# Kernel optimization log

Measured on AMD Instinct MI355X. Metric: run time of the kernel, lower is better.

Reference implementation:

```python
import jax, jax.numpy as jnp
import numpy as np

B, N, D, H = 4, 2048, 1024, 16
DK = D // H
LAMBDA = 0.5


def _linear_params(key, fan_in, fan_out):
    kw, kb = jax.random.split(key)
    bound = 1.0 / np.sqrt(fan_in)
    W = jax.random.uniform(kw, (fan_in, fan_out), jnp.float32, -bound, bound)
    b = jax.random.uniform(kb, (fan_out,), jnp.float32, -bound, bound)
    return W, b


def setup_inputs() -> dict:
    key = jax.random.key(0)
    ks = jax.random.split(key, 10)
    x = jax.random.normal(ks[0], (B, N, D), jnp.float32)
    # binary DAG-like adjacency (sparse-ish)
    causal_graph = jax.random.bernoulli(ks[1], 0.05, (N, N)).astype(jnp.float32)
    # differentiable backdoor mask: exp(-lambda*|Z|), 0 where no valid backdoor set
    Z = jax.random.randint(ks[2], (N, N), 0, 6).astype(jnp.float32)
    exists = jax.random.bernoulli(ks[3], 0.8, (N, N)).astype(jnp.float32)
    backdoor_mask = jnp.exp(-LAMBDA * Z) * exists
    Wq, bq = _linear_params(ks[4], D, D)
    Wk, bk = _linear_params(ks[5], D, D)
    Wc, bc = _linear_params(ks[6], N, D)  # W_cause: n_variables -> d_model
    We, be = _linear_params(ks[7], N, D)  # W_effect: n_variables -> d_model
    Wv, bv = _linear_params(ks[8], D, D)
    Wo, bo = _linear_params(ks[9], D, D)
    return dict(x=x, causal_graph=causal_graph, backdoor_mask=backdoor_mask,
                Wq=Wq, bq=bq, Wk=Wk, bk=bk, Wc=Wc, bc=bc, We=We, be=be,
                Wv=Wv, bv=bv, Wo=Wo, bo=bo)


def reference(x, causal_graph, backdoor_mask, Wq, bq, Wk, bk, Wc, bc, We, be, Wv, bv, Wo, bo):
    # Formula 5: asymmetric causal Q/K projections
    Q = x @ Wq + bq + (causal_graph @ Wc + bc)[None]        # [B,N,D]
    K = x @ Wk + bk + (causal_graph.T @ We + be)[None]      # [B,N,D]
    V = x @ Wv + bv                                          # [B,N,D]
    Qh = Q.reshape(B, N, H, DK)
    Kh = K.reshape(B, N, H, DK)
    Vh = V.reshape(B, N, H, DK)
    scores = jnp.einsum('bihd,bjhd->bhij', Qh, Kh) / np.sqrt(DK).astype(np.float32)
    # backdoor mask is MULTIPLICATIVE on raw scores (pre-softmax)
    scores = scores * backdoor_mask[None, None]
    attn = jax.nn.softmax(scores, axis=-1)                  # [B,H,N,N]
    out = jnp.einsum('bhij,bjhd->bihd', attn, Vh).reshape(B, N, D)
    return out @ Wo + bo
```

## Files before the change

### kernel.cpp

```cpp
#include <hip/hip_runtime.h>
#include <hip/hip_bf16.h>

#define BB 4
#define NN 2048
#define DD 1024
#define HH 16

using bf16 = __hip_bfloat16;
typedef __attribute__((ext_vector_type(8))) short bf16x8s;
typedef __attribute__((ext_vector_type(4))) float f32x4;

#define GLOAD_LDS16(gp, lp)                                                   \
  __builtin_amdgcn_global_load_lds(                                           \
      (const __attribute__((address_space(1))) void*)(gp),                    \
      (__attribute__((address_space(3))) void*)(lp), 16, 0, 0)

__global__ void cast_f32_bf16(const float* __restrict__ in, bf16* __restrict__ out, int n) {
  int i = (blockIdx.x * blockDim.x + threadIdx.x) * 4;
  if (i >= n) return;
  float4 v = *reinterpret_cast<const float4*>(in + i);
  ushort4 o;
  bf16 t0 = __float2bfloat16(v.x); o.x = *reinterpret_cast<unsigned short*>(&t0);
  bf16 t1 = __float2bfloat16(v.y); o.y = *reinterpret_cast<unsigned short*>(&t1);
  bf16 t2 = __float2bfloat16(v.z); o.z = *reinterpret_cast<unsigned short*>(&t2);
  bf16 t3 = __float2bfloat16(v.w); o.w = *reinterpret_cast<unsigned short*>(&t3);
  *reinterpret_cast<ushort4*>(out + i) = o;
}

__device__ __forceinline__ void transpose_tile(const float* __restrict__ in,
                                               bf16* __restrict__ out, int R, int C) {
  __shared__ float t[32][33];
  int c0 = blockIdx.x * 32, r0 = blockIdx.y * 32;
  int tx = threadIdx.x, ty = threadIdx.y;
#pragma unroll
  for (int i = 0; i < 4; i++)
    t[ty + i * 8][tx] = in[(size_t)(r0 + ty + i * 8) * C + c0 + tx];
  __syncthreads();
#pragma unroll
  for (int i = 0; i < 4; i++)
    out[(size_t)(c0 + ty + i * 8) * R + r0 + tx] = __float2bfloat16(t[tx][ty + i * 8]);
}

__global__ void transpose_cast(const float* __restrict__ in, bf16* __restrict__ out, int R, int C) {
  transpose_tile(in, out, R, C);
}

__global__ void transpose_cast4(const float* __restrict__ W0, const float* __restrict__ W1,
                                const float* __restrict__ W2, const float* __restrict__ W3,
                                bf16* __restrict__ O0, bf16* __restrict__ O1,
                                bf16* __restrict__ O2, bf16* __restrict__ O3) {
  const float* in; bf16* out;
  switch (blockIdx.z) {
    case 0: in = W0; out = O0; break;
    case 1: in = W1; out = O1; break;
    case 2: in = W2; out = O2; break;
    default: in = W3; out = O3; break;
  }
  transpose_tile(in, out, DD, DD);
}

__global__ void transpose_v(const bf16* __restrict__ Vb, bf16* __restrict__ Vt) {
  __shared__ short t[32][33];
  int bh = blockIdx.z; int b = bh >> 4, h = bh & 15;
  int n0 = blockIdx.x * 32, d0 = blockIdx.y * 32;
  int tx = threadIdx.x, ty = threadIdx.y;
#pragma unroll
  for (int i = 0; i < 4; i++)
    t[ty + i * 8][tx] = reinterpret_cast<const short*>(Vb)[
        (size_t)(b * NN + n0 + ty + i * 8) * DD + h * 64 + d0 + tx];
  __syncthreads();
#pragma unroll
  for (int i = 0; i < 4; i++)
    reinterpret_cast<short*>(Vt)[(size_t)(bh * 64 + d0 + ty + i * 8) * NN + n0 + tx] =
        t[tx][ty + i * 8];
}

template <int OUT_BF16, int HAS_ROWADD>
__device__ __forceinline__ void gemm_tile(
    const bf16* __restrict__ A, const bf16* __restrict__ BT, void* __restrict__ Cout,
    const float* __restrict__ bias, const float* __restrict__ rowadd,
    int Nc, int K, float scale, int brow, int bcol, short* As, short* Bs) {
  const int tid = threadIdx.x;
  const int l = tid & 63, w = tid >> 6;
  const int wr = (w >> 1) * 64, wc = (w & 1) * 64;
  const int lr = l & 15, lg = l >> 4;
  const int swz = lr & 7;
  f32x4 acc[4][4] = {};
  for (int k0 = 0; k0 < K; k0 += 64) {
#pragma unroll
    for (int i = 0; i < 4; i++) {
      int c = i * 256 + tid;
      int row = c >> 3, gch = (c & 7) ^ (row & 7);
      short* lA = As + (size_t)(i * 256 + w * 64) * 8;
      GLOAD_LDS16(A + (size_t)(brow + row) * K + k0 + gch * 8, lA);
      short* lB = Bs + (size_t)(i * 256 + w * 64) * 8;
      GLOAD_LDS16(BT + (size_t)(bcol + row) * K + k0 + gch * 8, lB);
    }
    __syncthreads();
#pragma unroll
    for (int t = 0; t < 2; t++) {
      bf16x8s a[4], bfr[4];
#pragma unroll
      for (int m = 0; m < 4; m++)
        a[m] = *reinterpret_cast<const bf16x8s*>(
            &As[(wr + m * 16 + lr) * 64 + ((t * 4 + lg) ^ swz) * 8]);
#pragma unroll
      for (int n = 0; n < 4; n++)
        bfr[n] = *reinterpret_cast<const bf16x8s*>(
            &Bs[(wc + n * 16 + lr) * 64 + ((t * 4 + lg) ^ swz) * 8]);
#pragma unroll
      for (int m = 0; m < 4; m++)
#pragma unroll
        for (int n = 0; n < 4; n++)
          acc[m][n] = __builtin_amdgcn_mfma_f32_16x16x32_bf16(a[m], bfr[n], acc[m][n], 0, 0, 0);
    }
    __syncthreads();
  }
#pragma unroll
  for (int m = 0; m < 4; m++) {
#pragma unroll
    for (int n = 0; n < 4; n++) {
      int col = bcol + wc + n * 16 + lr;
      float bv = bias[col];
#pragma unroll
      for (int r = 0; r < 4; r++) {
        int row = brow + wr + m * 16 + lg * 4 + r;
        float v = acc[m][n][r] + bv;
        if (HAS_ROWADD) v += rowadd[(size_t)(row & (NN - 1)) * Nc + col];
        v *= scale;
        if (OUT_BF16)
          reinterpret_cast<bf16*>(Cout)[(size_t)row * Nc + col] = __float2bfloat16(v);
        else
          reinterpret_cast<float*>(Cout)[(size_t)row * Nc + col] = v;
      }
    }
  }
}

template <int OUT_BF16, int HAS_ROWADD>
__global__ __launch_bounds__(256) void gemm_bt(
    const bf16* __restrict__ A, const bf16* __restrict__ BT, void* __restrict__ Cout,
    const float* __restrict__ bias, const float* __restrict__ rowadd,
    int M, int Nc, int K, float scale) {
  __shared__ short As[128 * 64];
  __shared__ short Bs[128 * 64];
  const int nbx = gridDim.x;
  const int nwg = nbx * gridDim.y;
  const int wg = blockIdx.y * nbx + blockIdx.x;
  const int swg = (wg & 7) * (nwg >> 3) + (wg >> 3);
  const int bxi = swg % nbx, byi = swg / nbx;
  gemm_tile<OUT_BF16, HAS_ROWADD>(A, BT, Cout, bias, rowadd, Nc, K, scale,
                                  byi * 128, bxi * 128, As, Bs);
}

__global__ __launch_bounds__(256) void gemm_dual(
    const bf16* __restrict__ A0, const bf16* __restrict__ B0, float* __restrict__ C0,
    const float* __restrict__ bias0,
    const bf16* __restrict__ A1, const bf16* __restrict__ B1, float* __restrict__ C1,
    const float* __restrict__ bias1, int Nc, int K) {
  __shared__ short As[128 * 64];
  __shared__ short Bs[128 * 64];
  const int nbx = gridDim.x;
  const int nwg = nbx * gridDim.y;
  const int wg = blockIdx.y * nbx + blockIdx.x;
  const int swg = (wg & 7) * (nwg >> 3) + (wg >> 3);
  const int bxi = swg % nbx, byi = swg / nbx;
  if (blockIdx.z == 0)
    gemm_tile<0, 0>(A0, B0, C0, bias0, nullptr, Nc, K, 1.0f, byi * 128, bxi * 128, As, Bs);
  else
    gemm_tile<0, 0>(A1, B1, C1, bias1, nullptr, Nc, K, 1.0f, byi * 128, bxi * 128, As, Bs);
}

__global__ __launch_bounds__(512, 4) void attn_k(
    const bf16* __restrict__ Qb, const bf16* __restrict__ Kb, const bf16* __restrict__ Vt,
    const float* __restrict__ mask, bf16* __restrict__ Ob) {
  constexpr int PPAD = 72;
  __shared__ short Ks[64 * 64];
  __shared__ short Vts[64 * 64];
  __shared__ short Ps[8][16 * PPAD];
  const int tid = threadIdx.x;
  const int wg = blockIdx.x;
  const int x = wg & 7, i = wg >> 3;
  const int b = x >> 1;
  const int h = ((x & 1) << 3) | (i & 7);
  const int q0 = ((i >> 3) & 15) * 128;
  const int l = tid & 63, w = tid >> 6;
  const int lr = l & 15, lg = l >> 4, lk = lg * 8;
  const int swz = lr & 7;

  const size_t qoff = (size_t)(b * NN + q0 + w * 16 + lr) * DD + h * 64;
  bf16x8s qf0 = *reinterpret_cast<const bf16x8s*>(Qb + qoff + lk);
  bf16x8s qf1 = *reinterpret_cast<const bf16x8s*>(Qb + qoff + 32 + lk);

  f32x4 acc[4] = {};
  float mrun = -1e30f, lrun = 0.f;

  const size_t kbase = (size_t)b * NN * DD + h * 64;
  const size_t vbase = (size_t)(b * HH + h) * 64 * NN;
  const float* mptr = mask + (size_t)(q0 + w * 16 + lr) * NN + lg * 4;

  const int r0 = tid >> 3, ch0 = tid & 7;
  const bf16* kg0 = Kb + kbase + (size_t)r0 * DD + ch0 * 8;
  const bf16* vg0 = Vt + vbase + (size_t)r0 * NN + ch0 * 8;
  short* kw0 = &Ks[r0 * 64 + (ch0 ^ (r0 & 7)) * 8];
  short* vw0 = &Vts[r0 * 64 + (ch0 ^ (r0 & 7)) * 8];

  uint4 kr0, vr0;
  kr0 = *reinterpret_cast<const uint4*>(kg0);
  vr0 = *reinterpret_cast<const uint4*>(vg0);

  for (int jt = 0; jt < NN; jt += 64) {
    __syncthreads();
    *reinterpret_cast<uint4*>(kw0) = kr0;
    *reinterpret_cast<uint4*>(vw0) = vr0;
    float4 m0 = *reinterpret_cast<const float4*>(mptr + jt + 0);
    float4 m1 = *reinterpret_cast<const float4*>(mptr + jt + 16);
    float4 m2 = *reinterpret_cast<const float4*>(mptr + jt + 32);
    float4 m3 = *reinterpret_cast<const float4*>(mptr + jt + 48);
    if (jt + 64 < NN) {
      kr0 = *reinterpret_cast<const uint4*>(kg0 + (size_t)(jt + 64) * DD);
      vr0 = *reinterpret_cast<const uint4*>(vg0 + jt + 64);
    }
    __syncthreads();

    f32x4 s[4];
#pragma unroll
    for (int jj = 0; jj < 4; jj++) {
      bf16x8s k0 = *reinterpret_cast<const bf16x8s*>(
          &Ks[(jj * 16 + lr) * 64 + ((0 + lg) ^ swz) * 8]);
      bf16x8s k1 = *reinterpret_cast<const bf16x8s*>(
          &Ks[(jj * 16 + lr) * 64 + ((4 + lg) ^ swz) * 8]);
      f32x4 z = {0.f, 0.f, 0.f, 0.f};
      z = __builtin_amdgcn_mfma_f32_16x16x32_bf16(k0, qf0, z, 0, 0, 0);
      s[jj] = __builtin_amdgcn_mfma_f32_16x16x32_bf16(k1, qf1, z, 0, 0, 0);
    }

    float lv[4][4];
    lv[0][0] = s[0][0] * m0.x; lv[0][1] = s[0][1] * m0.y;
    lv[0][2] = s[0][2] * m0.z; lv[0][3] = s[0][3] * m0.w;
    lv[1][0] = s[1][0] * m1.x; lv[1][1] = s[1][1] * m1.y;
    lv[1][2] = s[1][2] * m1.z; lv[1][3] = s[1][3] * m1.w;
    lv[2][0] = s[2][0] * m2.x; lv[2][1] = s[2][1] * m2.y;
    lv[2][2] = s[2][2] * m2.z; lv[2][3] = s[2][3] * m2.w;
    lv[3][0] = s[3][0] * m3.x; lv[3][1] = s[3][1] * m3.y;
    lv[3][2] = s[3][2] * m3.z; lv[3][3] = s[3][3] * m3.w;

    float mx0 = fmaxf(fmaxf(lv[0][0], lv[0][1]), fmaxf(lv[0][2], lv[0][3]));
    float mx1 = fmaxf(fmaxf(lv[1][0], lv[1][1]), fmaxf(lv[1][2], lv[1][3]));
    float mx2 = fmaxf(fmaxf(lv[2][0], lv[2][1]), fmaxf(lv[2][2], lv[2][3]));
    float mx3 = fmaxf(fmaxf(lv[3][0], lv[3][1]), fmaxf(lv[3][2], lv[3][3]));
    float mx = fmaxf(fmaxf(mx0, mx1), fmaxf(mx2, mx3));
    mx = fmaxf(mx, __shfl_xor(mx, 16, 64));
    mx = fmaxf(mx, __shfl_xor(mx, 32, 64));

    if (__any(mx > mrun + 11.0f)) {
      float mnew = fmaxf(mrun, mx);
      float sc = __builtin_amdgcn_exp2f(mrun - mnew);
      mrun = mnew;
      lrun *= sc;
#pragma unroll
      for (int s4 = 0; s4 < 4; s4++)
#pragma unroll
        for (int r = 0; r < 4; r++) acc[s4][r] *= sc;
    }

    short* Pw = &Ps[w][0];
    float rs = 0.f;
#pragma unroll
    for (int jj = 0; jj < 4; jj++) {
      float p0 = __builtin_amdgcn_exp2f(lv[jj][0] - mrun);
      float p1 = __builtin_amdgcn_exp2f(lv[jj][1] - mrun);
      float p2 = __builtin_amdgcn_exp2f(lv[jj][2] - mrun);
      float p3 = __builtin_amdgcn_exp2f(lv[jj][3] - mrun);
      rs += (p0 + p1) + (p2 + p3);
      ushort4 pk;
      bf16 b0 = __float2bfloat16(p0); pk.x = *reinterpret_cast<unsigned short*>(&b0);
      bf16 b1 = __float2bfloat16(p1); pk.y = *reinterpret_cast<unsigned short*>(&b1);
      bf16 b2 = __float2bfloat16(p2); pk.z = *reinterpret_cast<unsigned short*>(&b2);
      bf16 b3 = __float2bfloat16(p3); pk.w = *reinterpret_cast<unsigned short*>(&b3);
      *reinterpret_cast<ushort4*>(&Pw[lr * PPAD + jj * 16 + lg * 4]) = pk;
    }
    rs += __shfl_xor(rs, 16, 64);
    rs += __shfl_xor(rs, 32, 64);
    lrun += rs;

    asm volatile("s_waitcnt lgkmcnt(0)" ::: "memory");
    __builtin_amdgcn_sched_barrier(0);

    bf16x8s pb0 = *reinterpret_cast<const bf16x8s*>(&Pw[lr * PPAD + lk]);
    bf16x8s pb1 = *reinterpret_cast<const bf16x8s*>(&Pw[lr * PPAD + 32 + lk]);
#pragma unroll
    for (int s4 = 0; s4 < 4; s4++) {
      bf16x8s v0 = *reinterpret_cast<const bf16x8s*>(
          &Vts[(s4 * 16 + lr) * 64 + ((0 + lg) ^ swz) * 8]);
      bf16x8s v1 = *reinterpret_cast<const bf16x8s*>(
          &Vts[(s4 * 16 + lr) * 64 + ((4 + lg) ^ swz) * 8]);
      acc[s4] = __builtin_amdgcn_mfma_f32_16x16x32_bf16(v0, pb0, acc[s4], 0, 0, 0);
      acc[s4] = __builtin_amdgcn_mfma_f32_16x16x32_bf16(v1, pb1, acc[s4], 0, 0, 0);
    }
  }

  float rl = __builtin_amdgcn_rcpf(lrun);
  const size_t orow = (size_t)(b * NN + q0 + w * 16 + lr) * DD + h * 64;
#pragma unroll
  for (int s4 = 0; s4 < 4; s4++) {
    ushort4 o;
    bf16 b0 = __float2bfloat16(acc[s4][0] * rl); o.x = *reinterpret_cast<unsigned short*>(&b0);
    bf16 b1 = __float2bfloat16(acc[s4][1] * rl); o.y = *reinterpret_cast<unsigned short*>(&b1);
    bf16 b2 = __float2bfloat16(acc[s4][2] * rl); o.z = *reinterpret_cast<unsigned short*>(&b2);
    bf16 b3 = __float2bfloat16(acc[s4][3] * rl); o.w = *reinterpret_cast<unsigned short*>(&b3);
    *reinterpret_cast<ushort4*>(reinterpret_cast<unsigned short*>(Ob) + orow + s4 * 16 + lg * 4) = o;
  }
}

extern "C" void kernel_launch(void* const* d_in, const int* in_sizes, int n_in,
                              void* d_out, int out_size, void* d_ws, size_t ws_size,
                              hipStream_t stream) {
  (void)in_sizes; (void)n_in; (void)out_size; (void)ws_size;
  const float* x    = (const float*)d_in[0];
  const float* cg   = (const float*)d_in[1];
  const float* mask = (const float*)d_in[2];
  const float* Wq   = (const float*)d_in[3];
  const float* bq   = (const float*)d_in[4];
  const float* Wk   = (const float*)d_in[5];
  const float* bk   = (const float*)d_in[6];
  const float* Wc   = (const float*)d_in[7];
  const float* bc   = (const float*)d_in[8];
  const float* We   = (const float*)d_in[9];
  const float* be   = (const float*)d_in[10];
  const float* Wv   = (const float*)d_in[11];
  const float* bv   = (const float*)d_in[12];
  const float* Wo   = (const float*)d_in[13];
  const float* bo   = (const float*)d_in[14];

  auto MB = [](size_t m) { return m << 20; };
  char* ws = (char*)d_ws;
  bf16* xb   = (bf16*)(ws + MB(0));
  bf16* WqT  = (bf16*)(ws + MB(16));
  bf16* WkT  = (bf16*)(ws + MB(18));
  bf16* WvT  = (bf16*)(ws + MB(20));
  bf16* WoT  = (bf16*)(ws + MB(22));
  float* cq  = (float*)(ws + MB(24));
  float* ck  = (float*)(ws + MB(32));
  bf16* Qb   = (bf16*)(ws + MB(40));
  bf16* Kb   = (bf16*)(ws + MB(56));
  bf16* Vb   = (bf16*)(ws + MB(72));
  bf16* Vt   = (bf16*)(ws + MB(88));
  bf16* Ob   = (bf16*)(ws + MB(72));
  bf16* WcT  = (bf16*)(ws + MB(40));
  bf16* WeT  = (bf16*)(ws + MB(44));
  bf16* cgb  = (bf16*)(ws + MB(48));
  bf16* cgT  = (bf16*)(ws + MB(56));

  cast_f32_bf16<<<dim3(BB * NN * DD / 4 / 256), 256, 0, stream>>>(x, xb, BB * NN * DD);
  cast_f32_bf16<<<dim3(NN * NN / 4 / 256), 256, 0, stream>>>(cg, cgb, NN * NN);
  dim3 tb(32, 8);
  transpose_cast4<<<dim3(DD / 32, DD / 32, 4), tb, 0, stream>>>(
      Wq, Wk, Wv, Wo, WqT, WkT, WvT, WoT);
  transpose_cast<<<dim3(DD / 32, NN / 32), tb, 0, stream>>>(Wc, WcT, NN, DD);
  transpose_cast<<<dim3(DD / 32, NN / 32), tb, 0, stream>>>(We, WeT, NN, DD);
  transpose_cast<<<dim3(NN / 32, NN / 32), tb, 0, stream>>>(cg, cgT, NN, NN);

  gemm_dual<<<dim3(DD / 128, NN / 128, 2), 256, 0, stream>>>(
      cgb, WcT, cq, bc, cgT, WeT, ck, be, DD, NN);
  gemm_bt<1, 1><<<dim3(DD / 128, BB * NN / 128), 256, 0, stream>>>(
      xb, WqT, Qb, bq, cq, BB * NN, DD, DD, 0.125f * 1.4426950408889634f);
  gemm_bt<1, 1><<<dim3(DD / 128, BB * NN / 128), 256, 0, stream>>>(
      xb, WkT, Kb, bk, ck, BB * NN, DD, DD, 1.0f);
  gemm_bt<1, 0><<<dim3(DD / 128, BB * NN / 128), 256, 0, stream>>>(
      xb, WvT, Vb, bv, nullptr, BB * NN, DD, DD, 1.0f);

  transpose_v<<<dim3(NN / 32, 2, BB * HH), tb, 0, stream>>>(Vb, Vt);

  attn_k<<<dim3(NN / 128 * HH * BB), 512, 0, stream>>>(Qb, Kb, Vt, mask, Ob);

  gemm_bt<0, 0><<<dim3(DD / 128, BB * NN / 128), 256, 0, stream>>>(
      Ob, WoT, (float*)d_out, bo, nullptr, BB * NN, DD, DD, 1.0f);
}
```

Before: 315.8 us.

## Double attention query tile per block and fuse causal-graph prep kernels

Attention blocks now run 1024 threads (16 waves) over 256 query rows. Each K/V tile loaded into LDS is therefore reused by twice as many waves, and half the threads stage K while the other half stage V. MFMA sections are wrapped in s_setprio to favour matrix issue. The preprocessing also fuses the causal-graph cast and its transpose into one kernel, and merges the two Wc/We transposes into a single launch. The risks are fewer blocks (512), which hurts load balance and tail, and register pressure under launch_bounds(1024, 8).

```diff
diff --git a/kernel.cpp b/kernel.cpp
--- a/kernel.cpp
+++ b/kernel.cpp
@@ -41,10 +41,6 @@
     out[(size_t)(c0 + ty + i * 8) * R + r0 + tx] = __float2bfloat16(t[tx][ty + i * 8]);
 }
 
-__global__ void transpose_cast(const float* __restrict__ in, bf16* __restrict__ out, int R, int C) {
-  transpose_tile(in, out, R, C);
-}
-
 __global__ void transpose_cast4(const float* __restrict__ W0, const float* __restrict__ W1,
                                 const float* __restrict__ W2, const float* __restrict__ W3,
                                 bf16* __restrict__ O0, bf16* __restrict__ O1,
@@ -57,6 +53,30 @@
     default: in = W3; out = O3; break;
   }
   transpose_tile(in, out, DD, DD);
+}
+
+__global__ void transpose_cast2(const float* __restrict__ W0, const float* __restrict__ W1,
+                                bf16* __restrict__ O0, bf16* __restrict__ O1) {
+  const float* in = blockIdx.z ? W1 : W0;
+  bf16* out = blockIdx.z ? O1 : O0;
+  transpose_tile(in, out, NN, DD);
+}
+
+__global__ void cg_prep(const float* __restrict__ in, bf16* __restrict__ outN,
+                        bf16* __restrict__ outT) {
+  __shared__ float t[32][33];
+  int c0 = blockIdx.x * 32, r0 = blockIdx.y * 32;
+  int tx = threadIdx.x, ty = threadIdx.y;
+#pragma unroll
+  for (int i = 0; i < 4; i++) {
+    float v = in[(size_t)(r0 + ty + i * 8) * NN + c0 + tx];
+    t[ty + i * 8][tx] = v;
+    outN[(size_t)(r0 + ty + i * 8) * NN + c0 + tx] = __float2bfloat16(v);
+  }
+  __syncthreads();
+#pragma unroll
+  for (int i = 0; i < 4; i++)
+    outT[(size_t)(c0 + ty + i * 8) * NN + r0 + tx] = __float2bfloat16(t[tx][ty + i * 8]);
 }
 
 __global__ void transpose_v(const bf16* __restrict__ Vb, bf16* __restrict__ Vt) {
@@ -171,19 +191,19 @@
     gemm_tile<0, 0>(A1, B1, C1, bias1, nullptr, Nc, K, 1.0f, byi * 128, bxi * 128, As, Bs);
 }
 
-__global__ __launch_bounds__(512, 4) void attn_k(
+__global__ __launch_bounds__(1024, 8) void attn_k(
     const bf16* __restrict__ Qb, const bf16* __restrict__ Kb, const bf16* __restrict__ Vt,
     const float* __restrict__ mask, bf16* __restrict__ Ob) {
   constexpr int PPAD = 72;
   __shared__ short Ks[64 * 64];
   __shared__ short Vts[64 * 64];
-  __shared__ short Ps[8][16 * PPAD];
+  __shared__ short Ps[16][16 * PPAD];
   const int tid = threadIdx.x;
   const int wg = blockIdx.x;
   const int x = wg & 7, i = wg >> 3;
   const int b = x >> 1;
   const int h = ((x & 1) << 3) | (i & 7);
-  const int q0 = ((i >> 3) & 15) * 128;
+  const int q0 = ((i >> 3) & 7) * 256;
   const int l = tid & 63, w = tid >> 6;
   const int lr = l & 15, lg = l >> 4, lk = lg * 8;
   const int swz = lr & 7;
@@ -199,31 +219,29 @@
   const size_t vbase = (size_t)(b * HH + h) * 64 * NN;
   const float* mptr = mask + (size_t)(q0 + w * 16 + lr) * NN + lg * 4;
 
-  const int r0 = tid >> 3, ch0 = tid & 7;
-  const bf16* kg0 = Kb + kbase + (size_t)r0 * DD + ch0 * 8;
-  const bf16* vg0 = Vt + vbase + (size_t)r0 * NN + ch0 * 8;
-  short* kw0 = &Ks[r0 * 64 + (ch0 ^ (r0 & 7)) * 8];
-  short* vw0 = &Vts[r0 * 64 + (ch0 ^ (r0 & 7)) * 8];
-
-  uint4 kr0, vr0;
-  kr0 = *reinterpret_cast<const uint4*>(kg0);
-  vr0 = *reinterpret_cast<const uint4*>(vg0);
+  const int sr = (tid & 511) >> 3, sch = tid & 7;
+  const bool isK = tid < 512;
+  const bf16* sg = isK ? (Kb + kbase + (size_t)sr * DD + sch * 8)
+                       : (Vt + vbase + (size_t)sr * NN + sch * 8);
+  const size_t sstride = isK ? (size_t)DD : (size_t)1;
+  short* sw = isK ? &Ks[sr * 64 + (sch ^ (sr & 7)) * 8]
+                  : &Vts[sr * 64 + (sch ^ (sr & 7)) * 8];
+
+  uint4 sreg = *reinterpret_cast<const uint4*>(sg);
 
   for (int jt = 0; jt < NN; jt += 64) {
     __syncthreads();
-    *reinterpret_cast<uint4*>(kw0) = kr0;
-    *reinterpret_cast<uint4*>(vw0) = vr0;
+    *reinterpret_cast<uint4*>(sw) = sreg;
     float4 m0 = *reinterpret_cast<const float4*>(mptr + jt + 0);
     float4 m1 = *reinterpret_cast<const float4*>(mptr + jt + 16);
     float4 m2 = *reinterpret_cast<const float4*>(mptr + jt + 32);
     float4 m3 = *reinterpret_cast<const float4*>(mptr + jt + 48);
-    if (jt + 64 < NN) {
-      kr0 = *reinterpret_cast<const uint4*>(kg0 + (size_t)(jt + 64) * DD);
-      vr0 = *reinterpret_cast<const uint4*>(vg0 + jt + 64);
-    }
+    if (jt + 64 < NN)
+      sreg = *reinterpret_cast<const uint4*>(sg + (size_t)(jt + 64) * sstride);
     __syncthreads();
 
     f32x4 s[4];
+    __builtin_amdgcn_s_setprio(1);
 #pragma unroll
     for (int jj = 0; jj < 4; jj++) {
       bf16x8s k0 = *reinterpret_cast<const bf16x8s*>(
@@ -234,6 +252,7 @@
       z = __builtin_amdgcn_mfma_f32_16x16x32_bf16(k0, qf0, z, 0, 0, 0);
       s[jj] = __builtin_amdgcn_mfma_f32_16x16x32_bf16(k1, qf1, z, 0, 0, 0);
     }
+    __builtin_amdgcn_s_setprio(0);
 
     float lv[4][4];
     lv[0][0] = s[0][0] * m0.x; lv[0][1] = s[0][1] * m0.y;
@@ -289,6 +308,7 @@
 
     bf16x8s pb0 = *reinterpret_cast<const bf16x8s*>(&Pw[lr * PPAD + lk]);
     bf16x8s pb1 = *reinterpret_cast<const bf16x8s*>(&Pw[lr * PPAD + 32 + lk]);
+    __builtin_amdgcn_s_setprio(1);
 #pragma unroll
     for (int s4 = 0; s4 < 4; s4++) {
       bf16x8s v0 = *reinterpret_cast<const bf16x8s*>(
@@ -298,6 +318,7 @@
       acc[s4] = __builtin_amdgcn_mfma_f32_16x16x32_bf16(v0, pb0, acc[s4], 0, 0, 0);
       acc[s4] = __builtin_amdgcn_mfma_f32_16x16x32_bf16(v1, pb1, acc[s4], 0, 0, 0);
     }
+    __builtin_amdgcn_s_setprio(0);
   }
 
   float rl = __builtin_amdgcn_rcpf(lrun);
@@ -353,13 +374,11 @@
   bf16* cgT  = (bf16*)(ws + MB(56));
 
   cast_f32_bf16<<<dim3(BB * NN * DD / 4 / 256), 256, 0, stream>>>(x, xb, BB * NN * DD);
-  cast_f32_bf16<<<dim3(NN * NN / 4 / 256), 256, 0, stream>>>(cg, cgb, NN * NN);
   dim3 tb(32, 8);
+  cg_prep<<<dim3(NN / 32, NN / 32), tb, 0, stream>>>(cg, cgb, cgT);
   transpose_cast4<<<dim3(DD / 32, DD / 32, 4), tb, 0, stream>>>(
       Wq, Wk, Wv, Wo, WqT, WkT, WvT, WoT);
-  transpose_cast<<<dim3(DD / 32, NN / 32), tb, 0, stream>>>(Wc, WcT, NN, DD);
-  transpose_cast<<<dim3(DD / 32, NN / 32), tb, 0, stream>>>(We, WeT, NN, DD);
-  transpose_cast<<<dim3(NN / 32, NN / 32), tb, 0, stream>>>(cg, cgT, NN, NN);
+  transpose_cast2<<<dim3(DD / 32, NN / 32, 2), tb, 0, stream>>>(Wc, We, WcT, WeT);
 
   gemm_dual<<<dim3(DD / 128, NN / 128, 2), 256, 0, stream>>>(
       cgb, WcT, cq, bc, cgT, WeT, ck, be, DD, NN);
@@ -372,7 +391,7 @@
 
   transpose_v<<<dim3(NN / 32, 2, BB * HH), tb, 0, stream>>>(Vb, Vt);
 
-  attn_k<<<dim3(NN / 128 * HH * BB), 512, 0, stream>>>(Qb, Kb, Vt, mask, Ob);
+  attn_k<<<dim3(NN / 256 * HH * BB), 1024, 0, stream>>>(Qb, Kb, Vt, mask, Ob);
 
   gemm_bt<0, 0><<<dim3(DD / 128, BB * NN / 128), 256, 0, stream>>>(
       Ob, WoT, (float*)d_out, bo, nullptr, BB * NN, DD, DD, 1.0f);
```

Measured after the change: 563.9 us. 1.79x slower.
